# Kernel optimization log

Measured on AMD Instinct MI355X. Metric: run time of the kernel, lower is better.

The kernel has to match this reference:

```python
import jax, jax.numpy as jnp
import numpy as np

B, A, D = 2048, 8, 128          # batch, num_agents, obs_dims
G, HEADS = 128, 4               # gnn_output_dims, gnn_att_heads
H, MH = 128, 4                  # lstm hidden size, multihead-att heads
NL = 2                          # somu/scmu lstm layers
S = D + 2 * G                   # scmu input dims (obs concat 2 gnn layer outputs)
FC, ACT = 256, 14
FIN = S + (2 * NL + 1) * H + (2 * NL + 1) * H


def setup_inputs():
    key = jax.random.key(0)
    ctr = [0]
    def rn(shape, s=1.0):
        ctr[0] += 1
        return jax.random.normal(jax.random.fold_in(key, ctr[0]), shape, jnp.float32) * s
    w = 0.05
    inp = {
        'obs': rn((B, A, D)),
        'somu_h': rn((B, A, NL, H)), 'somu_c': rn((B, A, NL, H)),
        'scmu_h': rn((B, A, NL, H)), 'scmu_c': rn((B, A, NL, H)),
        'masks': jnp.ones((B, A, 1), jnp.float32),
    }
    for l, cin in ((0, D), (1, G)):
        inp[f'gnn_Wl{l}'] = rn((HEADS * G, cin), w)
        inp[f'gnn_bl{l}'] = jnp.zeros((HEADS * G,), jnp.float32)
        inp[f'gnn_Wr{l}'] = rn((HEADS * G, cin), w)
        inp[f'gnn_br{l}'] = jnp.zeros((HEADS * G,), jnp.float32)
        inp[f'gnn_att{l}'] = rn((HEADS, G), w)
        inp[f'gnn_bias{l}'] = jnp.zeros((G,), jnp.float32)
    for pre, cin in (('somu', D), ('scmu', S)):
        inp[f'{pre}_Wih0'] = rn((A, 4 * H, cin), w)
        inp[f'{pre}_Whh0'] = rn((A, 4 * H, H), w)
        inp[f'{pre}_bih0'] = jnp.zeros((A, 4 * H), jnp.float32)
        inp[f'{pre}_bhh0'] = jnp.zeros((A, 4 * H), jnp.float32)
        inp[f'{pre}_Wih1'] = rn((A, 4 * H, H), w)
        inp[f'{pre}_Whh1'] = rn((A, 4 * H, H), w)
        inp[f'{pre}_bih1'] = jnp.zeros((A, 4 * H), jnp.float32)
        inp[f'{pre}_bhh1'] = jnp.zeros((A, 4 * H), jnp.float32)
        inp[f'{pre}_qkv_w'] = rn((A, 3 * H, H), w)
        inp[f'{pre}_qkv_b'] = jnp.zeros((A, 3 * H), jnp.float32)
        inp[f'{pre}_out_w'] = rn((A, H, H), w)
        inp[f'{pre}_out_b'] = jnp.zeros((A, H), jnp.float32)
    inp['fc_w0'] = rn((FC, FIN), w); inp['fc_b0'] = jnp.zeros((FC,), jnp.float32)
    inp['fc_w1'] = rn((FC, FC), w); inp['fc_b1'] = jnp.zeros((FC,), jnp.float32)
    inp['act_w'] = rn((ACT, FC), w); inp['act_b'] = jnp.zeros((ACT,), jnp.float32)
    return inp


def _gatv2(x, Wl, bl, Wr, br, att, bias):
    # dense GATv2 over the complete agent graph (self-loops included)
    xl = (x @ Wl.T + bl).reshape(B, A, HEADS, G)
    xr = (x @ Wr.T + br).reshape(B, A, HEADS, G)
    s = xl[:, None, :, :, :] + xr[:, :, None, :, :]       # [B, tgt, src, h, G]
    e = jnp.einsum('bijhc,hc->bijh', jax.nn.leaky_relu(s, 0.2), att)
    alpha = jax.nn.softmax(e, axis=2)                      # softmax over sources
    out = jnp.einsum('bijh,bjhc->bihc', alpha, xl).mean(axis=2) + bias  # concat=False -> head mean
    return jax.nn.relu(out)


def _lstm_step(x, h, c, Wih, Whh, bih, bhh):
    g = x @ Wih.T + bih + h @ Whh.T + bhh
    i, f, gg, o = jnp.split(g, 4, axis=-1)                 # torch gate order i,f,g,o
    c2 = jax.nn.sigmoid(f) * c + jax.nn.sigmoid(i) * jnp.tanh(gg)
    return jax.nn.sigmoid(o) * jnp.tanh(c2), c2


def _mha(x, Wqkv, bqkv, Wo, bo):
    b, t, e = x.shape
    q, k, v = jnp.split(x @ Wqkv.T + bqkv, 3, axis=-1)
    dk = e // MH
    sp = lambda z: z.reshape(b, t, MH, dk).transpose(0, 2, 1, 3)
    q, k, v = sp(q), sp(k), sp(v)
    a = jax.nn.softmax(q @ k.transpose(0, 1, 3, 2) * np.float32(1.0 / np.sqrt(dk)), axis=-1)
    o = (a @ v).transpose(0, 2, 1, 3).reshape(b, t, e)
    return o @ Wo.T + bo


def reference(obs, somu_h, somu_c, scmu_h, scmu_c, masks,
              gnn_Wl0, gnn_bl0, gnn_Wr0, gnn_br0, gnn_att0, gnn_bias0,
              gnn_Wl1, gnn_bl1, gnn_Wr1, gnn_br1, gnn_att1, gnn_bias1,
              somu_Wih0, somu_Whh0, somu_bih0, somu_bhh0, somu_Wih1, somu_Whh1, somu_bih1, somu_bhh1,
              somu_qkv_w, somu_qkv_b, somu_out_w, somu_out_b,
              scmu_Wih0, scmu_Whh0, scmu_bih0, scmu_bhh0, scmu_Wih1, scmu_Whh1, scmu_bih1, scmu_bhh1,
              scmu_qkv_w, scmu_qkv_b, scmu_out_w, scmu_out_b,
              fc_w0, fc_b0, fc_w1, fc_b1, act_w, act_b):
    h1 = _gatv2(obs, gnn_Wl0, gnn_bl0, gnn_Wr0, gnn_br0, gnn_att0, gnn_bias0)
    h2 = _gatv2(h1, gnn_Wl1, gnn_bl1, gnn_Wr1, gnn_br1, gnn_att1, gnn_bias1)
    gnn_cat = jnp.concatenate([obs, h1, h2], axis=-1)      # [B, A, S]

    def agent(ob, gn, sh, sc, th, tc, m,
              sWih0, sWhh0, sbih0, sbhh0, sWih1, sWhh1, sbih1, sbhh1, sqw, sqb, sow, sob,
              tWih0, tWhh0, tbih0, tbhh0, tWih1, tWhh1, tbih1, tbhh1, tqw, tqb, tow, tob):
        mm = m[:, :, None]                                  # [B,1,1]: reset hidden state on mask=0
        sh, sc, th, tc = sh * mm, sc * mm, th * mm, tc * mm
        h0, c0 = _lstm_step(ob, sh[:, 0], sc[:, 0], sWih0, sWhh0, sbih0, sbhh0)
        h1_, c1_ = _lstm_step(h0, sh[:, 1], sc[:, 1], sWih1, sWhh1, sbih1, sbhh1)
        s_att = _mha(jnp.stack([h0, h1_, c0, c1_], axis=1), sqw, sqb, sow, sob).reshape(ob.shape[0], -1)
        g0, e0 = _lstm_step(gn, th[:, 0], tc[:, 0], tWih0, tWhh0, tbih0, tbhh0)
        g1, e1 = _lstm_step(g0, th[:, 1], tc[:, 1], tWih1, tWhh1, tbih1, tbhh1)
        t_att = _mha(jnp.stack([g0, g1, e0, e1], axis=1), tqw, tqb, tow, tob).reshape(ob.shape[0], -1)
        feat = jnp.concatenate([gn, h1_, s_att, g1, t_att], axis=-1)  # [B, FIN]
        x = jax.nn.relu(feat @ fc_w0.T + fc_b0)
        x = jax.nn.relu(x @ fc_w1.T + fc_b1)
        return jax.nn.log_softmax(x @ act_w.T + act_b, axis=-1)

    tr = lambda z: jnp.moveaxis(z, 1, 0)                    # [B,A,...] -> [A,B,...]
    out = jax.vmap(agent)(tr(obs), tr(gnn_cat), tr(somu_h), tr(somu_c), tr(scmu_h), tr(scmu_c), tr(masks),
                          somu_Wih0, somu_Whh0, somu_bih0, somu_bhh0, somu_Wih1, somu_Whh1, somu_bih1, somu_bhh1,
                          somu_qkv_w, somu_qkv_b, somu_out_w, somu_out_b,
                          scmu_Wih0, scmu_Whh0, scmu_bih0, scmu_bhh0, scmu_Wih1, scmu_Whh1, scmu_bih1, scmu_bhh1,
                          scmu_qkv_w, scmu_qkv_b, scmu_out_w, scmu_out_b)
    return jnp.moveaxis(out, 0, 1)                          # [B, A, ACT] action log-probs
```

## Files before the change

kernel.cpp:

```cpp
#include <hip/hip_runtime.h>
#include <math.h>

#define B_ 2048
#define A_ 8
#define ACT_ 14
#define FP_ 27262976l

typedef short short8 __attribute__((ext_vector_type(8)));
typedef float floatx4 __attribute__((ext_vector_type(4)));
typedef unsigned short u16x4 __attribute__((ext_vector_type(4)));

__device__ __forceinline__ unsigned short f2b(float f) {
    unsigned u = __float_as_uint(f);
    u += 0x7fff + ((u >> 16) & 1);
    return (unsigned short)(u >> 16);
}
__device__ __forceinline__ float b2f(unsigned short h) {
    return __uint_as_float(((unsigned)h) << 16);
}
__device__ __forceinline__ float sigm_(float x) { return 1.0f / (1.0f + __expf(-x)); }
__device__ __forceinline__ float tanh_(float x) { return 1.0f - 2.0f / (1.0f + __expf(2.0f * x)); }

struct GDesc {
    const unsigned short *X1, *X2, *W1, *W2;
    const float *b1, *b2;
    void* Y;
    const unsigned short* cms;
    unsigned short* tokp;
    unsigned short* featp;
    long xsa1, xsa2, wsa1, wps1, wsa2, wps2, bsa1, bsa2, ysa;
    int ldx1, K1, ldx2, K2, ldy, N, flags, nA, Nb, layer, foff;
};

#define LOADC(c, xh, whv, wlv) do {                                                       \
    const unsigned short *Xb_, *Wb_; int ldx_, K_, k0_; long wps_;                        \
    if ((c) < nC1) { Xb_ = X1; ldx_ = ldx1; K_ = K1; wps_ = wps1; Wb_ = W1; k0_ = (c) << 5; } \
    else { Xb_ = X2; ldx_ = ldx2; K_ = K2; wps_ = wps2; Wb_ = W2; k0_ = ((c) - nC1) << 5; } \
    _Pragma("unroll") for (int mi_ = 0; mi_ < MI; ++mi_) {                                \
        int row_ = xr0 + mi_ * 16 + lrow;                                                 \
        xh[mi_] = *(const short8*)(Xb_ + (long)(bm + row_) * ldx_ + k0_ + lslot * 8); }   \
    { int row_ = wr0 + lrow;                                                              \
      const unsigned short* wp_ = Wb_ + (long)(bn + row_) * K_ + k0_ + lslot * 8;         \
      whv = *(const short8*)wp_;                                                          \
      if (TT) wlv = *(const short8*)(wp_ + wps_); }                                       \
} while (0)

#define STOREC(P, xh, whv, wlv) do {                                                      \
    _Pragma("unroll") for (int mi_ = 0; mi_ < MI; ++mi_) {                                \
        int row_ = xr0 + mi_ * 16 + lrow; int sl_ = lslot ^ ((row_ >> 1) & 3);            \
        *(short8*)&Xh_l[P][row_ * 32 + sl_ * 8] = xh[mi_]; }                              \
    { int row_ = wr0 + lrow; int sl_ = lslot ^ ((row_ >> 1) & 3);                         \
      *(short8*)&Wh_l[P][row_ * 32 + sl_ * 8] = whv;                                      \
      if (TT) *(short8*)&Wl_l[P][row_ * 32 + sl_ * 8] = wlv; }                            \
} while (0)

#define COMPUTEC(P) do {                                                                  \
    short8 bh[4], bl[4];                                                                  \
    _Pragma("unroll") for (int ni = 0; ni < 4; ++ni) {                                    \
        int row_ = ni * 16 + lr; int off_ = row_ * 32 + ((lk ^ ((row_ >> 1) & 3)) * 8);   \
        bh[ni] = *(const short8*)&Wh_l[P][off_];                                          \
        if (TT) bl[ni] = *(const short8*)&Wl_l[P][off_]; }                                \
    _Pragma("unroll") for (int mi = 0; mi < MI; ++mi) {                                   \
        int row_ = xr0 + mi * 16 + lr; int off_ = row_ * 32 + ((lk ^ ((row_ >> 1) & 3)) * 8); \
        short8 ah = *(const short8*)&Xh_l[P][off_];                                       \
        _Pragma("unroll") for (int ni = 0; ni < 4; ++ni)                                  \
            acc[mi][ni] = __builtin_amdgcn_mfma_f32_16x16x32_bf16(ah, bh[ni], acc[mi][ni], 0, 0, 0); \
        if (TT) {                                                                         \
            _Pragma("unroll") for (int ni = 0; ni < 4; ++ni)                              \
                acc[mi][ni] = __builtin_amdgcn_mfma_f32_16x16x32_bf16(ah, bl[ni], acc[mi][ni], 0, 0, 0); \
        }                                                                                 \
    }                                                                                     \
} while (0)

template<int MI, int TT>
__launch_bounds__(256)
__global__ void mgemm_t(GDesc d)
{
    __shared__ __align__(16) unsigned short Xh_l[2][MI * 64 * 32];
    __shared__ __align__(16) unsigned short Wh_l[2][64 * 32];
    __shared__ __align__(16) unsigned short Wl_l[2][TT ? 64 * 32 : 8];

    const int wg = blockIdx.x;
    const unsigned short* X1 = d.X1; const unsigned short* X2 = d.X2;
    const unsigned short* W1 = d.W1; const unsigned short* W2 = d.W2;
    const float* b1 = d.b1; const float* b2 = d.b2;
    const long wps1 = d.wps1, wps2 = d.wps2, ysa = d.ysa;
    const int ldx1 = d.ldx1, K1 = d.K1, ldx2 = d.ldx2, K2 = d.K2;
    const int ldy = d.ldy, N = d.N, flags = d.flags, nA = d.nA, Nb = d.Nb;
    const int layer = d.layer, foff = d.foff;

    int a, mb, nb;
    if (nA == 8) { a = wg & 7; int q = wg >> 3; nb = q % Nb; mb = q / Nb; }
    else { a = 0; int x8 = wg & 7; int q = wg >> 3; nb = q % Nb; mb = (q / Nb) * 8 + x8; }

    X1 += (long)a * d.xsa1;
    W1 += (long)a * d.wsa1;
    if (X2) { X2 += (long)a * d.xsa2; W2 += (long)a * d.wsa2; }
    if (b1) b1 += (long)a * d.bsa1;
    if (b2) b2 += (long)a * d.bsa2;

    const int bm = mb * (MI * 64);
    const int bn = nb * 64;
    const int t = threadIdx.x;
    const int lane = t & 63, wid = t >> 6;

    floatx4 acc[MI][4] = {};

    const int xr0 = wid * (MI * 16);
    const int wr0 = wid * 16;
    const int lrow = lane >> 2;
    const int lslot = lane & 3;
    const int lr = lane & 15, lk = lane >> 4;

    const int nC1 = K1 >> 5;
    const int nC = nC1 + (X2 ? (K2 >> 5) : 0);

    short8 Axh[MI], Awh, Awl;
    short8 Bxh[MI], Bwh, Bwl;
    short8 Cxh[MI], Cwh, Cwl;
    short8 Dxh[MI], Dwh, Dwl;

    LOADC(0, Axh, Awh, Awl);
    if (nC > 1) LOADC(1, Bxh, Bwh, Bwl);
    if (nC > 2) LOADC(2, Cxh, Cwh, Cwl);
    if (nC > 3) LOADC(3, Dxh, Dwh, Dwl);

    for (int c = 0; c < nC; c += 4) {
        STOREC(0, Axh, Awh, Awl);
        __syncthreads();
        if (c + 4 < nC) LOADC(c + 4, Axh, Awh, Awl);
        COMPUTEC(0);
        if (c + 1 < nC) {
            STOREC(1, Bxh, Bwh, Bwl);
            __syncthreads();
            if (c + 5 < nC) LOADC(c + 5, Bxh, Bwh, Bwl);
            COMPUTEC(1);
        }
        if (c + 2 < nC) {
            STOREC(0, Cxh, Cwh, Cwl);
            __syncthreads();
            if (c + 6 < nC) LOADC(c + 6, Cxh, Cwh, Cwl);
            COMPUTEC(0);
        }
        if (c + 3 < nC) {
            STOREC(1, Dxh, Dwh, Dwl);
            __syncthreads();
            if (c + 7 < nC) LOADC(c + 7, Dxh, Dwh, Dwl);
            COMPUTEC(1);
        }
    }

    const int lg = lane >> 4;

    if (flags & 16) {
        const int j = (bn >> 2) + lr;
        unsigned short* tokp = d.tokp;
        unsigned short* featp = d.featp;
        const unsigned short* cms = d.cms;
#pragma unroll
        for (int mi = 0; mi < MI; ++mi) {
#pragma unroll
            for (int r = 0; r < 4; ++r) {
                const int b = bm + xr0 + mi * 16 + lg * 4 + r;
                float iv = acc[mi][0][r] + b1[j]       + b2[j];
                float fv = acc[mi][1][r] + b1[128 + j] + b2[128 + j];
                float gv = acc[mi][2][r] + b1[256 + j] + b2[256 + j];
                float ov = acc[mi][3][r] + b1[384 + j] + b2[384 + j];
                iv = sigm_(iv); fv = sigm_(fv); gv = tanh_(gv); ov = sigm_(ov);
                float cp = b2f(cms[(long)layer * 2097152 + (long)a * 262144 + b * 128 + j]);
                float c2 = fv * cp + iv * gv;
                float hv = ov * tanh_(c2);
                long tb = ((long)a * B_ + b) * 512;
                tokp[tb + layer * 128 + j] = f2b(hv);
                tokp[tb + (2 + layer) * 128 + j] = f2b(c2);
                if (featp) featp[((long)a * B_ + b) * 1664 + foff + j] = f2b(hv);
            }
        }
        return;
    }

    const bool relu = flags & 1, obf = flags & 2, fold = flags & 4, sbias = flags & 8;
    float* Yf = (float*)d.Y;
    unsigned short* Yh = (unsigned short*)d.Y;
#pragma unroll
    for (int mi = 0; mi < MI; ++mi) {
#pragma unroll
        for (int r = 0; r < 4; ++r) {
            int gm = bm + xr0 + mi * 16 + lg * 4 + r;
            long rowoff = fold ? ((long)(gm >> 2) * ldy + (gm & 3) * 128) : (long)gm * ldy;
            rowoff += (long)a * ysa;
#pragma unroll
            for (int ni = 0; ni < 4; ++ni) {
                int gc = bn + ni * 16 + lr;
                if (gc < N) {
                    float v = acc[mi][ni][r];
                    if (sbias) v += (gc < 512) ? b1[gc] : b2[gc - 512];
                    else { if (b1) v += b1[gc]; if (b2) v += b2[gc]; }
                    if (relu) v = fmaxf(v, 0.f);
                    if (obf) Yh[rowoff + gc] = f2b(v);
                    else     Yf[rowoff + gc] = v;
                }
            }
        }
    }
}

__launch_bounds__(512)
__global__ void sattn_k(const unsigned short* __restrict__ tokS,
                        const unsigned short* __restrict__ tokC,
                        const unsigned short* __restrict__ WqS,
                        const unsigned short* __restrict__ WqC,
                        const float* __restrict__ qbS, const float* __restrict__ qbC,
                        const unsigned short* __restrict__ WoS,
                        const unsigned short* __restrict__ WoC,
                        const float* __restrict__ obS, const float* __restrict__ obC,
                        unsigned short* __restrict__ feat)
{
    __shared__ __align__(16) unsigned short Xs[64 * 128];
    __shared__ __align__(16) unsigned short BufW[25600];
    __shared__ float qbias[384];
    __shared__ float obias[128];

    int bid = blockIdx.x;
    const unsigned short* tok; const unsigned short* Wq; const float* qb;
    const unsigned short* Wo; const float* ob; int foff;
    if (bid < 1024) { tok = tokS; Wq = WqS; qb = qbS; Wo = WoS; ob = obS; foff = 512; }
    else { bid -= 1024; tok = tokC; Wq = WqC; qb = qbC; Wo = WoC; ob = obC; foff = 1152; }

    const int a = bid & 7;
    const int g = bid >> 3;
    const int b0 = g * 16;

    const unsigned short* Wqa = Wq + (long)a * 49152;
    const unsigned short* Woa = Wo + (long)a * 16384;
    const unsigned short* tokb = tok + ((long)a * B_ + b0) * 512;

    const int t = threadIdx.x;
    const int lane = t & 63, wid = t >> 6;
    const int lr = lane & 15, lk = lane >> 4, lg = lane >> 4;

    int qwr[3], qws[3];
#pragma unroll
    for (int j = 0; j < 3; ++j) {
        int idx = t + j * 512;
        qwr[j] = idx >> 2; qws[j] = idx & 3;
    }
    const int owr = t >> 2, ows = t & 3;

    for (int idx = t; idx < 1024; idx += 512) {
        int r = idx >> 4, s = idx & 15;
        *(short8*)&Xs[r * 128 + (s ^ (r & 7)) * 8] = *(const short8*)(tokb + r * 128 + s * 8);
    }
    if (t < 384) qbias[t] = qb[a * 384 + t];
    if (t < 128) obias[t] = ob[a * 128 + t];

    unsigned short* Wh = BufW;

    short8 pw[3];
#pragma unroll
    for (int j = 0; j < 3; ++j)
        pw[j] = *(const short8*)(Wqa + qwr[j] * 128 + qws[j] * 8);

    floatx4 acc[4][3] = {};

    for (int kc = 0; kc < 4; ++kc) {
        const int k0 = kc * 32;
        if (kc) __syncthreads();
#pragma unroll
        for (int j = 0; j < 3; ++j) {
            unsigned short* dst = Wh + qwr[j] * 32 + ((qws[j] ^ ((qwr[j] >> 1) & 3)) * 8);
            *(short8*)dst = pw[j];
        }
        __syncthreads();
        if (kc < 3) {
            const int k1 = k0 + 32;
#pragma unroll
            for (int j = 0; j < 3; ++j)
                pw[j] = *(const short8*)(Wqa + qwr[j] * 128 + k1 + qws[j] * 8);
        }
        short8 af[4];
#pragma unroll
        for (int mi = 0; mi < 4; ++mi) {
            int row = mi * 16 + lr;
            int sl = ((k0 >> 3) + lk) ^ (row & 7);
            af[mi] = *(const short8*)&Xs[row * 128 + sl * 8];
        }
#pragma unroll
        for (int ni = 0; ni < 3; ++ni) {
            int nrow = wid * 48 + ni * 16 + lr;
            int off = nrow * 32 + ((lk ^ ((nrow >> 1) & 3)) * 8);
            short8 bh = *(const short8*)&Wh[off];
#pragma unroll
            for (int mi = 0; mi < 4; ++mi)
                acc[mi][ni] = __builtin_amdgcn_mfma_f32_16x16x32_bf16(af[mi], bh, acc[mi][ni], 0, 0, 0);
        }
    }
    __syncthreads();

    unsigned short* Q = BufW;
#pragma unroll
    for (int mi = 0; mi < 4; ++mi)
#pragma unroll
        for (int ni = 0; ni < 3; ++ni)
#pragma unroll
            for (int rr = 0; rr < 4; ++rr) {
                int row = mi * 16 + lg * 4 + rr;
                int col = wid * 48 + ni * 16 + lr;
                Q[row * 396 + col] = f2b(acc[mi][ni][rr] + qbias[col]);
            }
    __syncthreads();

    short8 po = *(const short8*)(Woa + owr * 128 + ows * 8);

    float oa[16];
    int qr, h4, hf;
    {
        int tt = t & 255;
        h4 = tt & 3; int tq = (tt >> 2) & 3, s = tt >> 4;
        hf = t >> 8;
        qr = s * 4 + tq;
        const unsigned short* qp = Q + qr * 396 + h4 * 32;
        float q[32];
#pragma unroll
        for (int r = 0; r < 8; ++r) {
            u16x4 v = *(const u16x4*)(qp + r * 4);
#pragma unroll
            for (int w = 0; w < 4; ++w) q[r * 4 + w] = b2f(v[w]);
        }
        float sv[4];
#pragma unroll
        for (int u = 0; u < 4; ++u) {
            const unsigned short* kp = Q + (s * 4 + u) * 396 + 128 + h4 * 32;
            float dd = 0.f;
#pragma unroll
            for (int r = 0; r < 8; ++r) {
                u16x4 v = *(const u16x4*)(kp + r * 4);
#pragma unroll
                for (int w = 0; w < 4; ++w) dd += q[r * 4 + w] * b2f(v[w]);
            }
            sv[u] = dd * 0.176776695296637f;
        }
        float mx = fmaxf(fmaxf(sv[0], sv[1]), fmaxf(sv[2], sv[3]));
        float e0 = __expf(sv[0] - mx), e1 = __expf(sv[1] - mx);
        float e2 = __expf(sv[2] - mx), e3 = __expf(sv[3] - mx);
        float inv = 1.0f / (e0 + e1 + e2 + e3);
        float al[4] = { e0 * inv, e1 * inv, e2 * inv, e3 * inv };
#pragma unroll
        for (int w = 0; w < 16; ++w) oa[w] = 0.f;
#pragma unroll
        for (int u = 0; u < 4; ++u) {
            const unsigned short* vp = Q + (s * 4 + u) * 396 + 256 + h4 * 32 + hf * 16;
            float wgt = al[u];
#pragma unroll
            for (int r = 0; r < 4; ++r) {
                u16x4 v = *(const u16x4*)(vp + r * 4);
#pragma unroll
                for (int w = 0; w < 4; ++w) oa[r * 4 + w] += wgt * b2f(v[w]);
            }
        }
    }
    __syncthreads();
    {
#pragma unroll
        for (int p = 0; p < 2; ++p) {
            short8 v;
#pragma unroll
            for (int w = 0; w < 8; ++w) v[w] = (short)f2b(oa[p * 8 + w]);
            int slot = h4 * 4 + hf * 2 + p;
            *(short8*)&Xs[qr * 128 + (slot ^ (qr & 7)) * 8] = v;
        }
    }

    unsigned short* Wh2 = BufW;
    floatx4 acc2[4] = {};

    for (int kc = 0; kc < 4; ++kc) {
        const int k0 = kc * 32;
        __syncthreads();
        {
            unsigned short* dst = Wh2 + owr * 32 + ((ows ^ ((owr >> 1) & 3)) * 8);
            *(short8*)dst = po;
        }
        __syncthreads();
        if (kc < 3) {
            const int k1 = k0 + 32;
            po = *(const short8*)(Woa + owr * 128 + k1 + ows * 8);
        }
        short8 af[4];
#pragma unroll
        for (int mi = 0; mi < 4; ++mi) {
            int row = mi * 16 + lr;
            int sl = ((k0 >> 3) + lk) ^ (row & 7);
            af[mi] = *(const short8*)&Xs[row * 128 + sl * 8];
        }
        {
            int nrow = wid * 16 + lr;
            int off = nrow * 32 + ((lk ^ ((nrow >> 1) & 3)) * 8);
            short8 bh = *(const short8*)&Wh2[off];
#pragma unroll
            for (int mi = 0; mi < 4; ++mi)
                acc2[mi] = __builtin_amdgcn_mfma_f32_16x16x32_bf16(af[mi], bh, acc2[mi], 0, 0, 0);
        }
    }

#pragma unroll
    for (int mi = 0; mi < 4; ++mi)
#pragma unroll
        for (int rr = 0; rr < 4; ++rr) {
            int row = mi * 16 + lg * 4 + rr;
            int s2 = row >> 2, tq2 = row & 3;
            long base = ((long)a * B_ + b0 + s2) * 1664 + foff + tq2 * 128;
            int col = wid * 16 + lr;
            feat[base + col] = f2b(acc2[mi][rr] + obias[col]);
        }
}

#define NW 19
struct WTab {
    const float* src[NW];
    long hoff[NW];
    long loff[NW];
    int n[NW];
    int npad[NW];
    int kc[NW];
    int wlo[NW];
};
__global__ void wcast_k(WTab tab, unsigned short* __restrict__ wb)
{
    const int e = blockIdx.y;
    const int np = tab.npad[e];
    const float* s = tab.src[e];
    unsigned short* dh = wb + tab.hoff[e];
    unsigned short* dl = wb + tab.loff[e];
    const int n = tab.n[e];
    const int kc = tab.kc[e];
    const int wlo = tab.wlo[e];
    for (long i = (long)blockIdx.x * 256 + threadIdx.x; i < np; i += (long)gridDim.x * 256) {
        long si = i;
        if (kc) {
            long per = 512l * kc;
            long ag = i / per;
            long rem = i - ag * per;
            int rp = (int)(rem / kc);
            int k = (int)(rem - (long)rp * kc);
            int srcr = (((rp & 63) >> 4) << 7) + ((rp >> 6) << 4) + (rp & 15);
            si = ag * per + (long)srcr * kc + k;
        }
        float v = (si < n) ? s[si] : 0.f;
        unsigned short h = f2b(v);
        dh[i] = h;
        if (wlo) dl[i] = f2b(v - b2f(h));
    }
}

__global__ void prep_k(const float* __restrict__ obs, const float* __restrict__ soh,
                       const float* __restrict__ sch, const float* __restrict__ soc,
                       const float* __restrict__ scc, const float* __restrict__ masks,
                       unsigned short* __restrict__ feat,
                       unsigned short* __restrict__ hmso, unsigned short* __restrict__ hmsc,
                       unsigned short* __restrict__ cmso, unsigned short* __restrict__ cmsc)
{
    long tid = (long)blockIdx.x * 256 + threadIdx.x;
    if (tid < 2097152) {
        int j = (int)(tid & 127);
        int row = (int)(tid >> 7);
        int b = row >> 3, aa = row & 7;
        feat[((long)aa * B_ + b) * 1664 + j] = f2b(obs[tid]);
        return;
    }
    long u = tid - 2097152;
    const float* src;
    unsigned short* dst;
    if (u < 4194304) { src = soh; dst = hmso; }
    else if (u < 2 * 4194304) { u -= 4194304; src = sch; dst = hmsc; }
    else if (u < 3 * 4194304) { u -= 2 * 4194304; src = soc; dst = cmso; }
    else { u -= 3 * 4194304; src = scc; dst = cmsc; }
    int j = (int)(u & 127);
    int b = (int)((u >> 7) & 2047);
    int aa = (int)((u >> 18) & 7);
    int l = (int)(u >> 21);
    float m = masks[b * 8 + aa];
    dst[u] = f2b(src[((long)(b * 8 + aa)) * 256 + l * 128 + j] * m);
}

__launch_bounds__(256)
__global__ void gat_reduce_k(const unsigned short* __restrict__ xlr,
                             const float* __restrict__ att, const float* __restrict__ bias,
                             unsigned short* __restrict__ feat, int coloff)
{
    __shared__ float xls[8][512];
    __shared__ float xrs[8][512];
    __shared__ float atts[512];
    __shared__ float es[8][8][4];
    __shared__ float as_[8][8][4];

    const int b = blockIdx.x;
    const int t = threadIdx.x;

    for (int i = t; i < 1024; i += 256) {
        int j = i >> 7, c4 = (i & 127) * 4;
        const unsigned short* base = xlr + ((long)j * B_ + b) * 1024;
        u16x4 vl = *(const u16x4*)(base + c4);
        u16x4 vr = *(const u16x4*)(base + 512 + c4);
#pragma unroll
        for (int q = 0; q < 4; ++q) {
            xls[j][c4 + q] = b2f(vl[q]);
            xrs[j][c4 + q] = b2f(vr[q]);
        }
    }
    for (int i = t; i < 128; i += 256)
        reinterpret_cast<float4*>(atts)[i] = reinterpret_cast<const float4*>(att)[i];
    __syncthreads();

    const int i = t >> 5, j = (t >> 2) & 7, h = t & 3;
    float e = 0.f;
    for (int cc = 0; cc < 128; ++cc) {
        int c = (cc + t) & 127;
        float s = xls[j][h * 128 + c] + xrs[i][h * 128 + c];
        s = s > 0.f ? s : 0.2f * s;
        e += s * atts[h * 128 + c];
    }
    es[i][j][h] = e;
    __syncthreads();

    float mx = -1e30f;
    for (int jj = 0; jj < 8; ++jj) mx = fmaxf(mx, es[i][jj][h]);
    float sum = 0.f;
    for (int jj = 0; jj < 8; ++jj) sum += __expf(es[i][jj][h] - mx);
    as_[i][j][h] = __expf(e - mx) / sum;
    __syncthreads();

    for (int idx = t; idx < 1024; idx += 256) {
        int ii = idx >> 7, c = idx & 127;
        float s = 0.f;
        for (int jj = 0; jj < 8; ++jj)
#pragma unroll
            for (int hh = 0; hh < 4; ++hh)
                s += as_[ii][jj][hh] * xls[jj][hh * 128 + c];
        s = s * 0.25f + bias[c];
        s = fmaxf(s, 0.f);
        feat[((long)ii * B_ + b) * 1664 + coloff + c] = f2b(s);
    }
}

__global__ void lsm_k(const float* __restrict__ logits, float* __restrict__ out)
{
    int tid = blockIdx.x * 256 + threadIdx.x;
    int b = tid & (B_ - 1);
    int a = tid >> 11;
    const float* lp = logits + ((long)a * B_ + b) * ACT_;
    float x[ACT_];
    float mx = -1e30f;
#pragma unroll
    for (int n = 0; n < ACT_; ++n) { x[n] = lp[n]; mx = fmaxf(mx, x[n]); }
    float sum = 0.f;
#pragma unroll
    for (int n = 0; n < ACT_; ++n) sum += __expf(x[n] - mx);
    float ls = mx + logf(sum);
    float* op = out + ((long)b * A_ + a) * ACT_;
#pragma unroll
    for (int n = 0; n < ACT_; ++n) op[n] = x[n] - ls;
}

extern "C" void kernel_launch(void* const* d_in, const int* in_sizes, int n_in,
                              void* d_out, int out_size, void* d_ws, size_t ws_size,
                              hipStream_t stream)
{
    const float* obs    = (const float*)d_in[0];
    const float* somu_h = (const float*)d_in[1];
    const float* somu_c = (const float*)d_in[2];
    const float* scmu_h = (const float*)d_in[3];
    const float* scmu_c = (const float*)d_in[4];
    const float* masks  = (const float*)d_in[5];
    const float* gWl0 = (const float*)d_in[6],  *gbl0 = (const float*)d_in[7];
    const float* gWr0 = (const float*)d_in[8],  *gbr0 = (const float*)d_in[9];
    const float* gatt0 = (const float*)d_in[10], *gbias0 = (const float*)d_in[11];
    const float* gWl1 = (const float*)d_in[12], *gbl1 = (const float*)d_in[13];
    const float* gWr1 = (const float*)d_in[14], *gbr1 = (const float*)d_in[15];
    const float* gatt1 = (const float*)d_in[16], *gbias1 = (const float*)d_in[17];
    const float* soWih0 = (const float*)d_in[18], *soWhh0 = (const float*)d_in[19];
    const float* sobih0 = (const float*)d_in[20], *sobhh0 = (const float*)d_in[21];
    const float* soWih1 = (const float*)d_in[22], *soWhh1 = (const float*)d_in[23];
    const float* sobih1 = (const float*)d_in[24], *sobhh1 = (const float*)d_in[25];
    const float* soqw = (const float*)d_in[26], *soqb = (const float*)d_in[27];
    const float* soow = (const float*)d_in[28], *soob = (const float*)d_in[29];
    const float* scWih0 = (const float*)d_in[30], *scWhh0 = (const float*)d_in[31];
    const float* scbih0 = (const float*)d_in[32], *scbhh0 = (const float*)d_in[33];
    const float* scWih1 = (const float*)d_in[34], *scWhh1 = (const float*)d_in[35];
    const float* scbih1 = (const float*)d_in[36], *scbhh1 = (const float*)d_in[37];
    const float* scqw = (const float*)d_in[38], *scqb = (const float*)d_in[39];
    const float* scow = (const float*)d_in[40], *scob = (const float*)d_in[41];
    const float* fcw0 = (const float*)d_in[42], *fcb0 = (const float*)d_in[43];
    const float* fcw1 = (const float*)d_in[44], *fcb1 = (const float*)d_in[45];
    const float* actw = (const float*)d_in[46], *actb = (const float*)d_in[47];

    unsigned short* wb = (unsigned short*)d_ws;
    long wo = 0;
    auto nxt = [&](long n) { long c = wo; wo += n; return c; };
    const long o_gW0 = nxt(262144), o_gW1 = nxt(262144);
    const long o_soWih0 = nxt(2 * 524288), o_soWhh0 = nxt(2 * 524288);
    const long o_soWih1 = nxt(2 * 524288), o_soWhh1 = nxt(2 * 524288);
    const long o_soqw = nxt(2 * 393216), o_soow = nxt(2 * 131072);
    const long o_scWih0 = nxt(2 * 1572864), o_scWhh0 = nxt(2 * 524288);
    const long o_scWih1 = nxt(2 * 524288), o_scWhh1 = nxt(2 * 524288);
    const long o_scqw = nxt(2 * 393216), o_scow = nxt(2 * 131072);
    const long o_fcw0 = nxt(2 * 425984), o_fcw1 = nxt(2 * 65536);
    const long o_actw = nxt(2 * 32768);

    unsigned short* feat   = wb + nxt(FP_);
    unsigned short* hmso   = wb + nxt(4194304);
    unsigned short* hmsc   = wb + nxt(4194304);
    unsigned short* cmso   = wb + nxt(4194304);
    unsigned short* cmsc   = wb + nxt(4194304);
    unsigned short* arenaA = wb + nxt(25165824);
    unsigned short* arenaB = wb + nxt(16777216);

    unsigned short* xlr    = arenaA;
    unsigned short* tokS   = arenaB;
    unsigned short* tokC   = arenaB + 8388608;
    unsigned short* x1     = arenaA;
    unsigned short* x2     = arenaA + 4194304;
    float*          logits = (float*)(arenaA + 8388608);

    WTab tab;
    int ei = 0;
    auto ent = [&](const float* s, long hoff, long loff, int n, int npad, int kc, int wlo) {
        tab.src[ei] = s; tab.hoff[ei] = hoff; tab.loff[ei] = loff;
        tab.n[ei] = n; tab.npad[ei] = npad; tab.kc[ei] = kc; tab.wlo[ei] = wlo; ++ei;
    };
    ent(gWl0, o_gW0,          o_gW0 + 131072,          65536, 65536, 0, 0);
    ent(gWr0, o_gW0 + 65536,  o_gW0 + 196608,          65536, 65536, 0, 0);
    ent(gWl1, o_gW1,          o_gW1 + 131072,          65536, 65536, 0, 0);
    ent(gWr1, o_gW1 + 65536,  o_gW1 + 196608,          65536, 65536, 0, 0);
    ent(soWih0, o_soWih0, o_soWih0 + 524288, 524288, 524288, 128, 0);
    ent(soWhh0, o_soWhh0, o_soWhh0 + 524288, 524288, 524288, 128, 0);
    ent(soWih1, o_soWih1, o_soWih1 + 524288, 524288, 524288, 128, 0);
    ent(soWhh1, o_soWhh1, o_soWhh1 + 524288, 524288, 524288, 128, 0);
    ent(soqw, o_soqw, o_soqw + 393216, 393216, 393216, 0, 0);
    ent(soow, o_soow, o_soow + 131072, 131072, 131072, 0, 0);
    ent(scWih0, o_scWih0, o_scWih0 + 1572864, 1572864, 1572864, 384, 0);
    ent(scWhh0, o_scWhh0, o_scWhh0 + 524288, 524288, 524288, 128, 0);
    ent(scWih1, o_scWih1, o_scWih1 + 524288, 524288, 524288, 128, 0);
    ent(scWhh1, o_scWhh1, o_scWhh1 + 524288, 524288, 524288, 128, 0);
    ent(scqw, o_scqw, o_scqw + 393216, 393216, 393216, 0, 0);
    ent(scow, o_scow, o_scow + 131072, 131072, 131072, 0, 0);
    ent(fcw0, o_fcw0, o_fcw0 + 425984, 425984, 425984, 0, 0);
    ent(fcw1, o_fcw1, o_fcw1 + 65536, 65536, 65536, 0, 0);
    ent(actw, o_actw, o_actw + 32768, 3584, 32768, 0, 1);
    wcast_k<<<dim3(1024, NW), 256, 0, stream>>>(tab, wb);

    prep_k<<<(2097152 + 4 * 4194304) / 256, 256, 0, stream>>>(
        obs, somu_h, scmu_h, somu_c, scmu_c, masks, feat, hmso, hmsc, cmso, cmsc);

    auto mkd = [&](const unsigned short* X1p, long xsa1, int ldx1, int K1,
                   const unsigned short* X2p, long xsa2, int ldx2, int K2,
                   long wo1, long wsa1, long wps1, long wo2, long wsa2, long wps2,
                   const float* bb1, long bsa1, const float* bb2, long bsa2,
                   void* Y, long ysa, int ldy, int N, int flags, int nA,
                   const unsigned short* cmsp, unsigned short* tokp, unsigned short* featp,
                   int layer, int foff) -> GDesc {
        GDesc d;
        d.X1 = X1p; d.X2 = X2p;
        d.W1 = wb + wo1; d.W2 = X2p ? wb + wo2 : nullptr;
        d.b1 = bb1; d.b2 = bb2; d.Y = Y;
        d.cms = cmsp; d.tokp = tokp; d.featp = featp;
        d.xsa1 = xsa1; d.xsa2 = xsa2;
        d.wsa1 = wsa1; d.wps1 = wps1; d.wsa2 = wsa2; d.wps2 = wps2;
        d.bsa1 = bsa1; d.bsa2 = bsa2; d.ysa = ysa;
        d.ldx1 = ldx1; d.K1 = K1; d.ldx2 = ldx2; d.K2 = K2; d.ldy = ldy; d.N = N;
        d.flags = flags; d.nA = nA; d.Nb = (N + 63) / 64;
        d.layer = layer; d.foff = foff;
        return d;
    };

    GDesc gat0 = mkd(feat, 0, 1664, 128, nullptr, 0, 0, 0,
                     o_gW0, 0, 131072, 0, 0, 0, gbl0, 0, gbr0, 0,
                     xlr, 0, 1024, 1024, 2 | 8, 1, nullptr, nullptr, nullptr, 0, 0);
    GDesc gat1 = mkd(feat + 128, 0, 1664, 128, nullptr, 0, 0, 0,
                     o_gW1, 0, 131072, 0, 0, 0, gbl1, 0, gbr1, 0,
                     xlr, 0, 1024, 1024, 2 | 8, 1, nullptr, nullptr, nullptr, 0, 0);
    GDesc so0  = mkd(feat, (long)B_ * 1664, 1664, 128, hmso, (long)B_ * 128, 128, 128,
                     o_soWih0, 512l * 128, 524288, o_soWhh0, 512l * 128, 524288,
                     sobih0, 512, sobhh0, 512, nullptr, 0, 0, 512, 16, A_,
                     cmso, tokS, nullptr, 0, 0);
    GDesc so1  = mkd(tokS, (long)B_ * 512, 512, 128, hmso + 2097152, (long)B_ * 128, 128, 128,
                     o_soWih1, 512l * 128, 524288, o_soWhh1, 512l * 128, 524288,
                     sobih1, 512, sobhh1, 512, nullptr, 0, 0, 512, 16, A_,
                     cmso, tokS, feat, 1, 384);
    GDesc sc0  = mkd(feat, (long)B_ * 1664, 1664, 384, hmsc, (long)B_ * 128, 128, 128,
                     o_scWih0, 512l * 384, 1572864, o_scWhh0, 512l * 128, 524288,
                     scbih0, 512, scbhh0, 512, nullptr, 0, 0, 512, 16, A_,
                     cmsc, tokC, nullptr, 0, 0);
    GDesc sc1  = mkd(tokC, (long)B_ * 512, 512, 128, hmsc + 2097152, (long)B_ * 128, 128, 128,
                     o_scWih1, 512l * 128, 524288, o_scWhh1, 512l * 128, 524288,
                     scbih1, 512, scbhh1, 512, nullptr, 0, 0, 512, 16, A_,
                     cmsc, tokC, feat, 1, 1024);
    GDesc fc0d = mkd(feat, 0, 1664, 1664, nullptr, 0, 0, 0,
                     o_fcw0, 0, 425984, 0, 0, 0, fcb0, 0, nullptr, 0,
                     x1, 0, 256, 256, 1 | 2, 1, nullptr, nullptr, nullptr, 0, 0);
    GDesc fc1d = mkd(x1, 0, 256, 256, nullptr, 0, 0, 0,
                     o_fcw1, 0, 65536, 0, 0, 0, fcb1, 0, nullptr, 0,
                     x2, 0, 256, 256, 1 | 2, 1, nullptr, nullptr, nullptr, 0, 0);
    GDesc actd = mkd(x2, 0, 256, 256, nullptr, 0, 0, 0,
                     o_actw, 0, 32768, 0, 0, 0, actb, 0, nullptr, 0,
                     logits, 0, ACT_, ACT_, 0, 1, nullptr, nullptr, nullptr, 0, 0);

    auto grid2 = [&](const GDesc& d, int M) { return d.nA * (M / 128) * d.Nb; };
    auto grid1 = [&](const GDesc& d, int M) { return d.nA * (M / 64) * d.Nb; };

    mgemm_t<2, 0><<<grid2(gat0, 16384), 256, 0, stream>>>(gat0);
    gat_reduce_k<<<B_, 256, 0, stream>>>(xlr, gatt0, gbias0, feat, 128);
    mgemm_t<2, 0><<<grid2(gat1, 16384), 256, 0, stream>>>(gat1);
    gat_reduce_k<<<B_, 256, 0, stream>>>(xlr, gatt1, gbias1, feat, 256);

    mgemm_t<1, 0><<<grid1(so0, B_), 256, 0, stream>>>(so0);
    mgemm_t<1, 0><<<grid1(so1, B_), 256, 0, stream>>>(so1);
    mgemm_t<1, 0><<<grid1(sc0, B_), 256, 0, stream>>>(sc0);
    mgemm_t<1, 0><<<grid1(sc1, B_), 256, 0, stream>>>(sc1);

    sattn_k<<<2048, 512, 0, stream>>>(tokS, tokC,
                                      wb + o_soqw, wb + o_scqw, soqb, scqb,
                                      wb + o_soow, wb + o_scow, soob, scob,
                                      feat);

    mgemm_t<2, 0><<<grid2(fc0d, 16384), 256, 0, stream>>>(fc0d);
    mgemm_t<2, 0><<<grid2(fc1d, 16384), 256, 0, stream>>>(fc1d);
    mgemm_t<2, 1><<<grid2(actd, 16384), 256, 0, stream>>>(actd);
    lsm_k<<<A_ * B_ / 256, 256, 0, stream>>>(logits, (float*)d_out);
}
```

Measured before the change: 334.3 us.

## Co-launch SOMU LSTM GEMMs with GAT GEMMs and double-buffer attention weights

The GEMM kernel now takes two descriptors and a block split index, so the SOMU layer-0 and layer-1 LSTM GEMMs run in the same launch as the GAT layer-0 and layer-1 projection GEMMs. Those SOMU GEMMs also switch from the 64-row tile variant to the 128-row variant. This is meant to cut launch count and fill the GPU better while the small LSTM grids run. Separately, the self-attention kernel double-buffers the QKV and output weight chunks in shared memory, dropping one barrier per k-step. In exchange it uses more shared memory and a larger, fully unrolled loop.

```diff
diff --git a/kernel.cpp b/kernel.cpp
--- a/kernel.cpp
+++ b/kernel.cpp
@@ -5,6 +5,7 @@
 #define A_ 8
 #define ACT_ 14
 #define FP_ 27262976l
+#define BIGSPLIT (1 << 30)
 
 typedef short short8 __attribute__((ext_vector_type(8)));
 typedef float floatx4 __attribute__((ext_vector_type(4)));
@@ -74,13 +75,16 @@
 
 template<int MI, int TT>
 __launch_bounds__(256)
-__global__ void mgemm_t(GDesc d)
+__global__ void mgemm_t(GDesc dA, GDesc dB, int split)
 {
     __shared__ __align__(16) unsigned short Xh_l[2][MI * 64 * 32];
     __shared__ __align__(16) unsigned short Wh_l[2][64 * 32];
     __shared__ __align__(16) unsigned short Wl_l[2][TT ? 64 * 32 : 8];
 
-    const int wg = blockIdx.x;
+    int wg = blockIdx.x;
+    GDesc d = dA;
+    if (wg >= split) { d = dB; wg -= split; }
+
     const unsigned short* X1 = d.X1; const unsigned short* X2 = d.X2;
     const unsigned short* W1 = d.W1; const unsigned short* W2 = d.W2;
     const float* b1 = d.b1; const float* b2 = d.b2;
@@ -254,29 +258,38 @@
     if (t < 384) qbias[t] = qb[a * 384 + t];
     if (t < 128) obias[t] = ob[a * 128 + t];
 
-    unsigned short* Wh = BufW;
+    unsigned short* Wh0 = BufW;
+    unsigned short* Wh1 = BufW + 12288;
 
     short8 pw[3];
 #pragma unroll
     for (int j = 0; j < 3; ++j)
         pw[j] = *(const short8*)(Wqa + qwr[j] * 128 + qws[j] * 8);
+#pragma unroll
+    for (int j = 0; j < 3; ++j)
+        *(short8*)(Wh0 + qwr[j] * 32 + ((qws[j] ^ ((qwr[j] >> 1) & 3)) * 8)) = pw[j];
+#pragma unroll
+    for (int j = 0; j < 3; ++j)
+        pw[j] = *(const short8*)(Wqa + qwr[j] * 128 + 32 + qws[j] * 8);
+
+    __syncthreads();
 
     floatx4 acc[4][3] = {};
 
+#pragma unroll
     for (int kc = 0; kc < 4; ++kc) {
         const int k0 = kc * 32;
-        if (kc) __syncthreads();
-#pragma unroll
-        for (int j = 0; j < 3; ++j) {
-            unsigned short* dst = Wh + qwr[j] * 32 + ((qws[j] ^ ((qwr[j] >> 1) & 3)) * 8);
-            *(short8*)dst = pw[j];
-        }
-        __syncthreads();
+        unsigned short* cur = (kc & 1) ? Wh1 : Wh0;
+        unsigned short* nxt = (kc & 1) ? Wh0 : Wh1;
         if (kc < 3) {
-            const int k1 = k0 + 32;
 #pragma unroll
             for (int j = 0; j < 3; ++j)
-                pw[j] = *(const short8*)(Wqa + qwr[j] * 128 + k1 + qws[j] * 8);
+                *(short8*)(nxt + qwr[j] * 32 + ((qws[j] ^ ((qwr[j] >> 1) & 3)) * 8)) = pw[j];
+            if (kc < 2) {
+#pragma unroll
+                for (int j = 0; j < 3; ++j)
+                    pw[j] = *(const short8*)(Wqa + qwr[j] * 128 + k0 + 64 + qws[j] * 8);
+            }
         }
         short8 af[4];
 #pragma unroll
@@ -289,13 +302,13 @@
         for (int ni = 0; ni < 3; ++ni) {
             int nrow = wid * 48 + ni * 16 + lr;
             int off = nrow * 32 + ((lk ^ ((nrow >> 1) & 3)) * 8);
-            short8 bh = *(const short8*)&Wh[off];
+            short8 bh = *(const short8*)&cur[off];
 #pragma unroll
             for (int mi = 0; mi < 4; ++mi)
                 acc[mi][ni] = __builtin_amdgcn_mfma_f32_16x16x32_bf16(af[mi], bh, acc[mi][ni], 0, 0, 0);
         }
-    }
-    __syncthreads();
+        __syncthreads();
+    }
 
     unsigned short* Q = BufW;
 #pragma unroll
@@ -360,6 +373,7 @@
         }
     }
     __syncthreads();
+
     {
 #pragma unroll
         for (int p = 0; p < 2; ++p) {
@@ -370,21 +384,22 @@
             *(short8*)&Xs[qr * 128 + (slot ^ (qr & 7)) * 8] = v;
         }
     }
-
-    unsigned short* Wh2 = BufW;
+    unsigned short* W20 = BufW;
+    unsigned short* W21 = BufW + 4096;
+    *(short8*)(W20 + owr * 32 + ((ows ^ ((owr >> 1) & 3)) * 8)) = po;
+    po = *(const short8*)(Woa + owr * 128 + 32 + ows * 8);
+    __syncthreads();
+
     floatx4 acc2[4] = {};
-
+#pragma unroll
     for (int kc = 0; kc < 4; ++kc) {
         const int k0 = kc * 32;
-        __syncthreads();
-        {
-            unsigned short* dst = Wh2 + owr * 32 + ((ows ^ ((owr >> 1) & 3)) * 8);
-            *(short8*)dst = po;
-        }
-        __syncthreads();
+        unsigned short* cur = (kc & 1) ? W21 : W20;
+        unsigned short* nxt = (kc & 1) ? W20 : W21;
         if (kc < 3) {
-            const int k1 = k0 + 32;
-            po = *(const short8*)(Woa + owr * 128 + k1 + ows * 8);
+            *(short8*)(nxt + owr * 32 + ((ows ^ ((owr >> 1) & 3)) * 8)) = po;
+            if (kc < 2)
+                po = *(const short8*)(Woa + owr * 128 + k0 + 64 + ows * 8);
         }
         short8 af[4];
 #pragma unroll
@@ -396,11 +411,12 @@
         {
             int nrow = wid * 16 + lr;
             int off = nrow * 32 + ((lk ^ ((nrow >> 1) & 3)) * 8);
-            short8 bh = *(const short8*)&Wh2[off];
+            short8 bh = *(const short8*)&cur[off];
 #pragma unroll
             for (int mi = 0; mi < 4; ++mi)
                 acc2[mi] = __builtin_amdgcn_mfma_f32_16x16x32_bf16(af[mi], bh, acc2[mi], 0, 0, 0);
         }
+        if (kc < 3) __syncthreads();
     }
 
 #pragma unroll
@@ -708,23 +724,27 @@
     auto grid2 = [&](const GDesc& d, int M) { return d.nA * (M / 128) * d.Nb; };
     auto grid1 = [&](const GDesc& d, int M) { return d.nA * (M / 64) * d.Nb; };
 
-    mgemm_t<2, 0><<<grid2(gat0, 16384), 256, 0, stream>>>(gat0);
+    {
+        int gA = grid2(gat0, 16384), gB = grid2(so0, B_);
+        mgemm_t<2, 0><<<gA + gB, 256, 0, stream>>>(gat0, so0, gA);
+    }
     gat_reduce_k<<<B_, 256, 0, stream>>>(xlr, gatt0, gbias0, feat, 128);
-    mgemm_t<2, 0><<<grid2(gat1, 16384), 256, 0, stream>>>(gat1);
+    {
+        int gA = grid2(gat1, 16384), gB = grid2(so1, B_);
+        mgemm_t<2, 0><<<gA + gB, 256, 0, stream>>>(gat1, so1, gA);
+    }
     gat_reduce_k<<<B_, 256, 0, stream>>>(xlr, gatt1, gbias1, feat, 256);
 
-    mgemm_t<1, 0><<<grid1(so0, B_), 256, 0, stream>>>(so0);
-    mgemm_t<1, 0><<<grid1(so1, B_), 256, 0, stream>>>(so1);
-    mgemm_t<1, 0><<<grid1(sc0, B_), 256, 0, stream>>>(sc0);
-    mgemm_t<1, 0><<<grid1(sc1, B_), 256, 0, stream>>>(sc1);
+    mgemm_t<1, 0><<<grid1(sc0, B_), 256, 0, stream>>>(sc0, sc0, BIGSPLIT);
+    mgemm_t<1, 0><<<grid1(sc1, B_), 256, 0, stream>>>(sc1, sc1, BIGSPLIT);
 
     sattn_k<<<2048, 512, 0, stream>>>(tokS, tokC,
                                       wb + o_soqw, wb + o_scqw, soqb, scqb,
                                       wb + o_soow, wb + o_scow, soob, scob,
                                       feat);
 
-    mgemm_t<2, 0><<<grid2(fc0d, 16384), 256, 0, stream>>>(fc0d);
-    mgemm_t<2, 0><<<grid2(fc1d, 16384), 256, 0, stream>>>(fc1d);
-    mgemm_t<2, 1><<<grid2(actd, 16384), 256, 0, stream>>>(actd);
+    mgemm_t<2, 0><<<grid2(fc0d, 16384), 256, 0, stream>>>(fc0d, fc0d, BIGSPLIT);
+    mgemm_t<2, 0><<<grid2(fc1d, 16384), 256, 0, stream>>>(fc1d, fc1d, BIGSPLIT);
+    mgemm_t<2, 1><<<grid2(actd, 16384), 256, 0, stream>>>(actd, actd, BIGSPLIT);
     lsm_k<<<A_ * B_ / 256, 256, 0, stream>>>(logits, (float*)d_out);
 }
```

Measured after the change: 322.8 us. 1.04x faster.
